# Performance work log

Hardware: AMD Instinct MI355X
Metric: run time of the kernel (lower is better)

## Reference

```python
import jax, jax.numpy as jnp
import numpy as np

EPS = 1e-6


def gaussian_filt(x, k, sigma):
    # x: [B,H,W,C]; depthwise gaussian conv with reflect padding, matching
    # TCFormer guassian_filt (kernel uses analytic 1/(2*pi*var) normalization).
    C = x.shape[-1]
    coords = jnp.arange(k, dtype=x.dtype)
    mean = (k - 1) / 2.0
    var = float(sigma) ** 2
    g1 = jnp.exp(-(coords - mean) ** 2 / (2.0 * var))
    gk = (g1[:, None] * g1[None, :]) / (2.0 * np.pi * var)  # [k,k]
    w = jnp.tile(gk[:, :, None, None], (1, 1, 1, C))  # HWIO, depthwise
    pad = (k - 1) // 2
    xp = jnp.pad(x, ((0, 0), (pad, pad), (pad, pad), (0, 0)), mode='reflect')
    return jax.lax.conv_general_dilated(
        xp, w, (1, 1), 'VALID',
        dimension_numbers=('NHWC', 'HWIO', 'NHWC'), feature_group_count=C)


def token2map(x, loc, H, W, kernel_size, sigma):
    # Scatter-mean tokens x [B,N,C] at normalized locations loc [B,N,2] in [-1,1]
    # onto an HxW grid, then gaussian-splat to fill holes. Returns NHWC map.
    B, N, C = x.shape
    loc = jnp.clip(loc, -1.0, 1.0)
    px = jnp.clip(jnp.round(0.5 * (loc[..., 0] + 1.0) * W - 0.5).astype(jnp.int32), 0, W - 1)
    py = jnp.clip(jnp.round(0.5 * (loc[..., 1] + 1.0) * H - 0.5).astype(jnp.int32), 0, H - 1)
    idx = py * W + px + jnp.arange(B, dtype=jnp.int32)[:, None] * (H * W)  # [B,N]
    src = jnp.concatenate([x, jnp.ones((B, N, 1), x.dtype)], axis=-1)  # [B,N,C+1]
    out = jnp.zeros((B * H * W, C + 1), x.dtype).at[idx.reshape(-1)].add(src.reshape(-1, C + 1))
    out = out.reshape(B, H, W, C + 1)
    feat, cnt = out[..., :C], out[..., C:]
    feat = feat / (cnt + EPS)
    mask = (cnt > 0).astype(x.dtype)
    feat = feat * mask
    if kernel_size > 1:
        # reconstruct_feature: fill empty cells with gaussian-interpolated values
        y = gaussian_filt(jnp.concatenate([feat, mask], axis=-1), kernel_size, sigma)
        fi, mi = y[..., :C], y[..., C:]
        fi = fi / (mi + EPS)
        fi = fi * (mi > 0).astype(x.dtype)
        feat = feat + (1.0 - mask) * fi
    return feat  # [B,H,W,C]


def layernorm(x, g, b, eps=1e-5):
    m = jnp.mean(x, axis=-1, keepdims=True)
    v = jnp.var(x, axis=-1, keepdims=True)
    return (x - m) / jnp.sqrt(v + eps) * g + b


def setup_inputs() -> dict:
    key = jax.random.key(0)
    ks = jax.random.split(key, 8)
    B, N, C, H, W = 8, 16384, 64, 128, 128
    SR = 8
    std = 0.02
    return {
        'x': jax.random.normal(ks[0], (B, N, C), jnp.float32),
        'x_source': jax.random.normal(ks[1], (B, N, C), jnp.float32),
        'loc_source': jax.random.uniform(ks[2], (B, N, 2), jnp.float32) * 2.0 - 1.0,
        'conf_source': jax.random.normal(ks[3], (B, N, 1), jnp.float32) * 0.1,
        'q_w': jax.random.normal(ks[4], (C, C), jnp.float32) * std,
        'kv_w': jax.random.normal(ks[5], (2 * C, C), jnp.float32) * std,
        'sr_w': jax.random.normal(ks[6], (SR, SR, C, C), jnp.float32) * np.sqrt(2.0 / (SR * SR * C)),
        'sr_b': jnp.zeros((C,), jnp.float32),
        'norm_w': jnp.ones((C,), jnp.float32),
        'norm_b': jnp.zeros((C,), jnp.float32),
        'proj_w': jax.random.normal(ks[7], (C, C), jnp.float32) * std,
        'proj_b': jnp.zeros((C,), jnp.float32),
        'H': H,
        'W': W,
    }


def reference(x, x_source, loc_source, conf_source, q_w, kv_w, sr_w, sr_b,
              norm_w, norm_b, proj_w, proj_b, H, W):
    B, N, C = x.shape
    num_heads = 1  # PVT stage-1
    hd = C // num_heads
    scale = hd ** -0.5
    sr = sr_w.shape[0]  # sr_ratio = 8

    # q projection: [B, nh, N, hd]
    q = (x @ q_w.T).reshape(B, N, num_heads, hd).transpose(0, 2, 1, 3)

    # token2map scatter-splat (kernel = sr_ratio + 1, sigma = 2)
    feat = token2map(x_source, loc_source, H, W, sr + 1, 2.0)  # [B,H,W,C]

    # SR conv (k = stride = sr_ratio), then layernorm
    xs = jax.lax.conv_general_dilated(
        feat, sr_w, (sr, sr), 'VALID',
        dimension_numbers=('NHWC', 'HWIO', 'NHWC')) + sr_b
    h, w = H // sr, W // sr
    xs = layernorm(xs.reshape(B, h * w, C), norm_w, norm_b)  # [B,M,C]

    # confidence map on the reduced grid (kernel_size=1 => pure scatter-mean)
    conf = token2map(conf_source, loc_source, h, w, 1, 1.0).reshape(B, h * w)  # [B,M]

    kv = (xs @ kv_w.T).reshape(B, h * w, 2, num_heads, hd)
    k = kv[:, :, 0].transpose(0, 2, 1, 3)  # [B,nh,M,hd]
    v = kv[:, :, 1].transpose(0, 2, 1, 3)

    attn = jnp.einsum('bhnd,bhmd->bhnm', q, k) * scale
    attn = attn + conf[:, None, None, :]  # additive confidence bias
    attn = jax.nn.softmax(attn, axis=-1)
    out = jnp.einsum('bhnm,bhmd->bhnd', attn, v)
    out = out.transpose(0, 2, 1, 3).reshape(B, N, C)
    return out @ proj_w.T + proj_b
```

## Files before the change

### kernel.cpp

```cpp
#include <hip/hip_runtime.h>
#include <hip/hip_bf16.h>

#define NN 16384
#define NC 64
#define GH 128
#define GW 128
#define GM 256

typedef __attribute__((ext_vector_type(8))) short bf16x8;
typedef __attribute__((ext_vector_type(4))) float f32x4;

static __device__ __forceinline__ int reflect128(int i){
  if (i < 0) i = -i;
  if (i > 127) i = 254 - i;
  return i;
}

static __device__ __forceinline__ ushort f2bf(float f){
  __hip_bfloat16 h = __float2bfloat16(f);
  union { __hip_bfloat16 h; ushort u; } v; v.h = h;
  return v.u;
}

static __device__ __forceinline__ int cell_of(float l, float S2, int hi){
  l = fminf(fmaxf(l, -1.f), 1.f);
  float u = l + 1.f;
  int p = (int)rintf(u*S2 - 0.5f);
  return min(max(p,0),hi);
}

__global__ __launch_bounds__(256) void k_zero(float4* __restrict__ p, int n4){
  int i = blockIdx.x*256 + threadIdx.x;
  int stride = gridDim.x*256;
  float4 z = make_float4(0.f,0.f,0.f,0.f);
  for (; i < n4; i += stride) p[i] = z;
}

__global__ __launch_bounds__(256) void k_scatter_feat(
    const float* __restrict__ xsrc, const float* __restrict__ loc,
    float* __restrict__ featg){
  int gid = blockIdx.x*256 + threadIdx.x;
  int t = gid >> 6;
  int b = t >> 14;
  int px = cell_of(loc[2*t],   64.f, 127);
  int py = cell_of(loc[2*t+1], 64.f, 127);
  int cell = (b*GH + py)*GW + px;
  atomicAdd(&featg[cell*NC + (gid & 63)], xsrc[gid]);
}

__global__ __launch_bounds__(256) void k_scatter_aux(
    const float* __restrict__ loc, const float* __restrict__ csrc,
    float* __restrict__ cnt, float* __restrict__ csum, float* __restrict__ ccnt){
  int t = blockIdx.x*256 + threadIdx.x;
  int b = t >> 14;
  int px = cell_of(loc[2*t],   64.f, 127);
  int py = cell_of(loc[2*t+1], 64.f, 127);
  atomicAdd(&cnt[(b*GH+py)*GW+px], 1.0f);
  int qx = cell_of(loc[2*t],   8.f, 15);
  int qy = cell_of(loc[2*t+1], 8.f, 15);
  int cell = b*GM + qy*16 + qx;
  atomicAdd(&csum[cell], csrc[t]);
  atomicAdd(&ccnt[cell], 1.0f);
}

__global__ __launch_bounds__(256) void k_finalize_feat(
    float* __restrict__ featg, const float* __restrict__ cnt){
  int gid = blockIdx.x*256 + threadIdx.x;
  float cn = cnt[gid>>6];
  float v  = featg[gid];
  featg[gid] = (cn > 0.f) ? v/(cn+1e-6f) : 0.f;
}

__global__ __launch_bounds__(256) void k_finalize_conf(
    const float* __restrict__ csum, const float* __restrict__ ccnt,
    float* __restrict__ conf){
  int i = blockIdx.x*256 + threadIdx.x;
  float cn = ccnt[i];
  conf[i] = (cn > 0.f) ? csum[i]/(cn+1e-6f) : 0.f;
}

__global__ __launch_bounds__(256) void k_fill2(
    const float* __restrict__ cnt, float* __restrict__ feat){
  int gid = blockIdx.x*256 + threadIdx.x;
  int p = gid >> 2, cg = gid & 3;
  if (cnt[p] > 0.f) return;
  int b = p>>14, py=(p>>7)&127, px=p&127;
  const float fn = 0.039788735772973836f;
  float g1[9];
  #pragma unroll
  for (int i=0;i<9;++i){ float d=(float)i-4.f; g1[i]=__expf(-d*d*0.125f); }
  float4 acc[4];
  #pragma unroll
  for (int i=0;i<4;++i) acc[i]=make_float4(0.f,0.f,0.f,0.f);
  float msum=0.f;
  for (int dy=0; dy<9; ++dy){
    int iy = reflect128(py-4+dy);
    for (int dx=0; dx<9; ++dx){
      int ix = reflect128(px-4+dx);
      int q  = (b*GH+iy)*GW+ix;
      if (cnt[q] <= 0.f) continue;
      float wn = g1[dy]*g1[dx]*fn;
      msum += wn;
      const float4* fr = (const float4*)&feat[q*NC + cg*16];
      #pragma unroll
      for (int k=0;k<4;++k){
        float4 vv = fr[k];
        acc[k].x += wn*vv.x; acc[k].y += wn*vv.y;
        acc[k].z += wn*vv.z; acc[k].w += wn*vv.w;
      }
    }
  }
  if (msum <= 0.f) return;
  float inv = 1.f/(msum + 1e-6f);
  float4* o = (float4*)&feat[p*NC + cg*16];
  #pragma unroll
  for (int k=0;k<4;++k)
    o[k] = make_float4(acc[k].x*inv, acc[k].y*inv, acc[k].z*inv, acc[k].w*inv);
}

static __device__ __forceinline__ int rowswz(int bid){
  return ((bid & 7) << 7) + (bid >> 3);
}

__global__ __launch_bounds__(256) void k_finfillh(
    float* __restrict__ feat, const float* __restrict__ cnt,
    float* __restrict__ feath, float* __restrict__ maskh){
  __shared__ float F[GW*NC];
  __shared__ float CR[GW];
  int py = rowswz(blockIdx.x), t = threadIdx.x;
  const float fn = 0.039788735772973836f;
  float g1n[9];
  #pragma unroll
  for (int i=0;i<9;++i){ float d=(float)i-4.f; g1n[i]=__expf(-d*d*0.125f)*fn; }
  if (t < GW) CR[t] = cnt[py*GW + t];
  __syncthreads();
  for (int i=t*4; i<GW*NC; i+=1024){
    int px = i>>6;
    float cn = CR[px];
    float inv = (cn > 0.f) ? 1.f/(cn+1e-6f) : 0.f;
    float4 v = *(const float4*)&feat[(size_t)py*GW*NC + i];
    v.x*=inv; v.y*=inv; v.z*=inv; v.w*=inv;
    *(float4*)&F[i] = v;
    *(float4*)&feat[(size_t)py*GW*NC + i] = v;
  }
  __syncthreads();
  for (int i=t*4; i<GW*NC; i+=1024){
    int px = i>>6, c = i&63;
    float4 acc = make_float4(0.f,0.f,0.f,0.f);
    #pragma unroll
    for (int dx=0; dx<9; ++dx){
      int ix = reflect128(px-4+dx);
      float w = g1n[dx];
      float4 v = *(const float4*)&F[ix*NC + c];
      acc.x += w*v.x; acc.y += w*v.y; acc.z += w*v.z; acc.w += w*v.w;
    }
    *(float4*)&feath[(size_t)py*GW*NC + i] = acc;
  }
  if (t < GW){
    float hm = 0.f;
    #pragma unroll
    for (int dx=0; dx<9; ++dx){
      int ix = reflect128(t-4+dx);
      hm += g1n[dx]*((CR[ix] > 0.f) ? 1.f : 0.f);
    }
    maskh[py*GW + t] = hm;
  }
}

__global__ __launch_bounds__(256) void k_fillv(
    float* __restrict__ feat, const float* __restrict__ cnt,
    const float* __restrict__ feath, const float* __restrict__ maskh){
  int pyg = rowswz(blockIdx.x), t = threadIdx.x;
  int b = pyg >> 7, pyl = pyg & 127;
  int px = t>>1, c0 = (t&1)<<5;
  float g1[9];
  #pragma unroll
  for (int i=0;i<9;++i){ float d=(float)i-4.f; g1[i]=__expf(-d*d*0.125f); }
  float cn = cnt[pyg*GW + px];
  float ym = 0.f;
  int ry[9];
  #pragma unroll
  for (int dy=0; dy<9; ++dy){
    ry[dy] = b*GH + reflect128(pyl-4+dy);
    ym += g1[dy]*maskh[ry[dy]*GW + px];
  }
  if (cn > 0.f || ym <= 0.f) return;
  float inv = 1.f/(ym + 1e-6f);
  float4 acc[8];
  #pragma unroll
  for (int k=0;k<8;++k) acc[k]=make_float4(0.f,0.f,0.f,0.f);
  #pragma unroll
  for (int dy=0; dy<9; ++dy){
    float w = g1[dy];
    const float4* hf = (const float4*)&feath[((size_t)ry[dy]*GW+px)*NC + c0];
    #pragma unroll
    for (int k=0;k<8;++k){
      float4 v = hf[k];
      acc[k].x += w*v.x; acc[k].y += w*v.y; acc[k].z += w*v.z; acc[k].w += w*v.w;
    }
  }
  float4* o = (float4*)&feat[((size_t)pyg*GW+px)*NC + c0];
  #pragma unroll
  for (int k=0;k<8;++k)
    o[k] = make_float4(acc[k].x*inv, acc[k].y*inv, acc[k].z*inv, acc[k].w*inv);
}

__global__ __launch_bounds__(256) void k_srconv(
    const float* __restrict__ feat, const float* __restrict__ srw,
    float* __restrict__ xs0){
  alignas(16) __shared__ float A[64*65];
  alignas(16) __shared__ float Bs[64*64];
  int mt = blockIdx.x, kh = blockIdx.y;
  int t = threadIdx.x;
  int tm = t>>4, tn = t&15;
  float acc[4][4] = {{0.f}};
  for (int kc=0; kc<8; ++kc){
    __syncthreads();
    for (int idx=t; idx<4096; idx+=256){
      int mr = idx>>6, kk = idx&63;
      int m = mt*64+mr;
      int b = m>>8, oh=(m>>4)&15, ow=m&15;
      A[mr*65+kk] = feat[(((b*GH)+(oh*8+kh))*GW + ow*8)*NC + kc*64 + kk];
    }
    for (int idx=t; idx<4096; idx+=256)
      Bs[idx] = srw[(kh*512 + kc*64)*64 + idx];
    __syncthreads();
    for (int kk=0; kk<64; ++kk){
      float4 bv = *(const float4*)&Bs[kk*64 + tn*4];
      #pragma unroll
      for (int i=0;i<4;++i){
        float av = A[(tm*4+i)*65 + kk];
        acc[i][0] += av*bv.x; acc[i][1] += av*bv.y;
        acc[i][2] += av*bv.z; acc[i][3] += av*bv.w;
      }
    }
  }
  #pragma unroll
  for (int i=0;i<4;++i)
    #pragma unroll
    for (int j=0;j<4;++j)
      atomicAdd(&xs0[(mt*64+tm*4+i)*64 + tn*4+j], acc[i][j]);
}

__global__ __launch_bounds__(256) void k_srconv2(
    const float* __restrict__ feat, const float* __restrict__ srw,
    float* __restrict__ part){
  alignas(16) __shared__ float A[64*65];
  alignas(16) __shared__ float Bs[64*64];
  int mt = blockIdx.x, kh = blockIdx.y, kq = blockIdx.z;
  int t = threadIdx.x;
  int tm = t>>4, tn = t&15;
  float acc[4][4] = {{0.f}};
  for (int kc=0; kc<4; ++kc){
    int kw = kq*4 + kc;
    __syncthreads();
    for (int idx=t; idx<4096; idx+=256){
      int mr = idx>>6, kk = idx&63;
      int m = mt*64+mr;
      int b = m>>8, oh=(m>>4)&15, ow=m&15;
      A[mr*65+kk] = feat[(((b*GH)+(oh*8+kh))*GW + ow*8 + kw)*NC + kk];
    }
    for (int idx=t; idx<4096; idx+=256)
      Bs[idx] = srw[(kh*512 + kw*64)*64 + idx];
    __syncthreads();
    for (int kk=0; kk<64; ++kk){
      float4 bv = *(const float4*)&Bs[kk*64 + tn*4];
      #pragma unroll
      for (int i=0;i<4;++i){
        float av = A[(tm*4+i)*65 + kk];
        acc[i][0] += av*bv.x; acc[i][1] += av*bv.y;
        acc[i][2] += av*bv.z; acc[i][3] += av*bv.w;
      }
    }
  }
  float* pdst = part + (size_t)(kh*2+kq)*2048*64;
  #pragma unroll
  for (int i=0;i<4;++i)
    #pragma unroll
    for (int j=0;j<4;++j)
      pdst[(mt*64+tm*4+i)*64 + tn*4+j] = acc[i][j];
}

__global__ __launch_bounds__(256) void k_ln(
    const float* __restrict__ xs0, const float* __restrict__ srb,
    const float* __restrict__ nw, const float* __restrict__ nbv,
    float* __restrict__ xs){
  int row  = blockIdx.x*4 + (threadIdx.x>>6);
  int lane = threadIdx.x & 63;
  float v = xs0[row*64+lane] + srb[lane];
  float s = v;
  #pragma unroll
  for (int off=32; off; off>>=1) s += __shfl_xor(s, off, 64);
  float mean = s*(1.f/64.f);
  float d = v - mean;
  float s2 = d*d;
  #pragma unroll
  for (int off=32; off; off>>=1) s2 += __shfl_xor(s2, off, 64);
  float var = s2*(1.f/64.f);
  xs[row*64+lane] = d*(1.f/sqrtf(var+1e-5f))*nw[lane] + nbv[lane];
}

__global__ __launch_bounds__(256) void k_kv1(
    const float* __restrict__ xs, const float* __restrict__ kvw,
    float* __restrict__ kraw, float* __restrict__ vraw){
  int gid = blockIdx.x*256 + threadIdx.x;
  int r = gid >> 6, d = gid & 63;
  const float* xr = &xs[r*64];
  float ka=0.f, va=0.f;
  for (int c=0;c<64;++c){
    float xc = xr[c];
    ka += xc*kvw[d*64+c];
    va += xc*kvw[(64+d)*64+c];
  }
  kraw[gid] = ka;
  vraw[gid] = va;
}

__global__ __launch_bounds__(256) void k_kvproj2(
    const float* __restrict__ kraw, const float* __restrict__ vraw,
    const float* __restrict__ qw, const float* __restrict__ pw,
    ushort* __restrict__ KB, ushort* __restrict__ VB){
  int gid = blockIdx.x*256 + threadIdx.x;
  int r = gid >> 6, c = gid & 63;
  int b = r >> 8, m = r & 255;
  const float* kr = &kraw[r*64];
  const float* vr = &vraw[r*64];
  float ak=0.f, av=0.f;
  for (int i=0;i<64;++i){
    ak += kr[i]*qw[i*64+c];
    av += vr[i]*pw[c*64+i];
  }
  {
    int nt = m>>4, l15 = m&15, kb = c>>5, h = (c>>3)&3, j = c&7;
    KB[((((b*16 + nt)*2 + kb)*4 + h)*16 + l15)*8 + j] = f2bf(ak);
  }
  {
    int ct = c>>4, n15 = c&15, kb2 = m>>5, h2 = (m>>3)&3, j2 = m&7;
    VB[((((b*4 + ct)*8 + kb2)*4 + h2)*16 + n15)*8 + j2] = f2bf(av);
  }
}

__global__ __launch_bounds__(256) void k_kvfused(
    const float* __restrict__ part, const float* __restrict__ srb,
    const float* __restrict__ nw, const float* __restrict__ nbv,
    const float* __restrict__ kvw, const float* __restrict__ qw,
    const float* __restrict__ pw,
    ushort* __restrict__ KB, ushort* __restrict__ VB){
  __shared__ float XR[4][64], KR[4][64], VR[4][64];
  int t = threadIdx.x;
  int rl = t>>6, d = t&63;
  int r  = blockIdx.x*4 + rl;
  float v = srb[d];
  #pragma unroll
  for (int ps=0; ps<16; ++ps)
    v += part[(size_t)ps*2048*64 + r*64 + d];
  float s = v;
  #pragma unroll
  for (int off=32; off; off>>=1) s += __shfl_xor(s, off, 64);
  float mean = s*(1.f/64.f);
  float dd = v - mean;
  float s2 = dd*dd;
  #pragma unroll
  for (int off=32; off; off>>=1) s2 += __shfl_xor(s2, off, 64);
  float var = s2*(1.f/64.f);
  XR[rl][d] = dd*(1.f/sqrtf(var+1e-5f))*nw[d] + nbv[d];
  __syncthreads();
  float ka=0.f, va=0.f;
  for (int cc=0; cc<64; ++cc){
    float xc = XR[rl][cc];
    ka += xc*kvw[d*64+cc];
    va += xc*kvw[(64+d)*64+cc];
  }
  KR[rl][d] = ka; VR[rl][d] = va;
  __syncthreads();
  int c = d;
  float ak=0.f, av=0.f;
  for (int i=0;i<64;++i){
    ak += KR[rl][i]*qw[i*64+c];
    av += VR[rl][i]*pw[c*64+i];
  }
  int b = r>>8, m = r&255;
  {
    int nt = m>>4, l15 = m&15, kb = c>>5, h = (c>>3)&3, j = c&7;
    KB[((((b*16 + nt)*2 + kb)*4 + h)*16 + l15)*8 + j] = f2bf(ak);
  }
  {
    int ct = c>>4, n15 = c&15, kb2 = m>>5, h2 = (m>>3)&3, j2 = m&7;
    VB[((((b*4 + ct)*8 + kb2)*4 + h2)*16 + n15)*8 + j2] = f2bf(av);
  }
}

__global__ __launch_bounds__(256) void k_attn5(
    const float* __restrict__ x, const ushort* __restrict__ KB,
    const ushort* __restrict__ VB, const float* __restrict__ conf,
    const float* __restrict__ projb, float* __restrict__ out){
  alignas(16) __shared__ ushort P[4*4096];
  int t = threadIdx.x, w = t>>6, l = t&63;
  int b = blockIdx.x >> 8;
  int row0 = ((blockIdx.x & 255) << 6) + (w<<4);
  int l15 = l & 15, h = l >> 4;
  const ushort* KBb = KB + b*16384;
  const ushort* VBb = VB + b*16384;
  bf16x8 xa[2];
  {
    const float* xr = x + (size_t)(b*NN + row0 + l15)*64 + h*8;
    #pragma unroll
    for (int kb=0; kb<2; ++kb){
      float4 a0 = *(const float4*)(xr + 32*kb);
      float4 a1 = *(const float4*)(xr + 32*kb + 4);
      bf16x8 v;
      v[0]=(short)f2bf(a0.x); v[1]=(short)f2bf(a0.y);
      v[2]=(short)f2bf(a0.z); v[3]=(short)f2bf(a0.w);
      v[4]=(short)f2bf(a1.x); v[5]=(short)f2bf(a1.y);
      v[6]=(short)f2bf(a1.z); v[7]=(short)f2bf(a1.w);
      xa[kb]=v;
    }
  }
  f32x4 acc[16];
  #pragma unroll
  for (int nt=0;nt<16;++nt) acc[nt] = (f32x4){0.f,0.f,0.f,0.f};
  #pragma unroll
  for (int nt=0;nt<16;++nt){
    bf16x8 b0 = *(const bf16x8*)(KBb + (nt*2+0)*512 + l*8);
    bf16x8 b1 = *(const bf16x8*)(KBb + (nt*2+1)*512 + l*8);
    acc[nt] = __builtin_amdgcn_mfma_f32_16x16x32_bf16(xa[0], b0, acc[nt], 0,0,0);
    acc[nt] = __builtin_amdgcn_mfma_f32_16x16x32_bf16(xa[1], b1, acc[nt], 0,0,0);
  }
  float rs[4] = {0.f,0.f,0.f,0.f};
  ushort* Pw = P + w*4096;
  #pragma unroll
  for (int nt=0;nt<16;++nt){
    float cf = conf[b*GM + nt*16 + l15];
    #pragma unroll
    for (int reg=0;reg<4;++reg){
      float p = __expf(fmaf(acc[nt][reg], 0.125f, cf));
      rs[reg] += p;
      int m   = nt*16 + l15;
      int row = h*4 + reg;
      int ld  = ((m>>3)&3)*16 + row;
      int idx = ((m>>5)*512 + ld*8 + (m&7)) ^ (ld & 0x38);
      Pw[idx] = f2bf(p);
    }
  }
  #pragma unroll
  for (int off=1; off<16; off<<=1){
    #pragma unroll
    for (int reg=0;reg<4;++reg) rs[reg] += __shfl_xor(rs[reg], off, 64);
  }
  f32x4 oacc[4];
  #pragma unroll
  for (int ct=0;ct<4;++ct) oacc[ct] = (f32x4){0.f,0.f,0.f,0.f};
  #pragma unroll
  for (int kb2=0;kb2<8;++kb2){
    int ridx = (kb2*512 + l*8) ^ (l & 0x38);
    bf16x8 pa = *(const bf16x8*)(Pw + ridx);
    #pragma unroll
    for (int ct=0;ct<4;++ct){
      bf16x8 vb = *(const bf16x8*)(VBb + (ct*8+kb2)*512 + l*8);
      oacc[ct] = __builtin_amdgcn_mfma_f32_16x16x32_bf16(pa, vb, oacc[ct], 0,0,0);
    }
  }
  float* OT = (float*)Pw;
  #pragma unroll
  for (int ct=0;ct<4;++ct){
    float pb4 = projb[ct*16 + l15];
    #pragma unroll
    for (int reg=0;reg<4;++reg)
      OT[(h*4+reg)*68 + ct*16 + l15] = oacc[ct][reg]/rs[reg] + pb4;
  }
  #pragma unroll
  for (int i=0;i<4;++i){
    int row = i*4 + h;
    float4 v = *(const float4*)&OT[row*68 + l15*4];
    *(float4*)&out[(size_t)(b*NN + row0 + row)*64 + l15*4] = v;
  }
}

__global__ __launch_bounds__(256) void k_attn6(
    const float* __restrict__ x, const ushort* __restrict__ KB,
    const ushort* __restrict__ VB, const float* __restrict__ conf,
    const float* __restrict__ projb, float* __restrict__ out){
  alignas(16) __shared__ ushort P[4*4096];
  int t = threadIdx.x, w = t>>6, l = t&63;
  int b = blockIdx.x >> 8;
  int row0 = ((blockIdx.x & 255) << 6) + (w<<4);
  int l15 = l & 15, h = l >> 4;
  const ushort* KBb = KB + b*16384;
  const ushort* VBb = VB + b*16384;

  bf16x8 xa[2];
  {
    const float* xr = x + (size_t)(b*NN + row0 + l15)*64 + h*8;
    #pragma unroll
    for (int kb=0; kb<2; ++kb){
      float4 a0 = *(const float4*)(xr + 32*kb);
      float4 a1 = *(const float4*)(xr + 32*kb + 4);
      bf16x8 v;
      v[0]=(short)f2bf(a0.x); v[1]=(short)f2bf(a0.y);
      v[2]=(short)f2bf(a0.z); v[3]=(short)f2bf(a0.w);
      v[4]=(short)f2bf(a1.x); v[5]=(short)f2bf(a1.y);
      v[6]=(short)f2bf(a1.z); v[7]=(short)f2bf(a1.w);
      xa[kb]=v;
    }
  }

  float rs[4] = {0.f,0.f,0.f,0.f};
  f32x4 oacc[4];
  #pragma unroll
  for (int ct=0;ct<4;++ct) oacc[ct] = (f32x4){0.f,0.f,0.f,0.f};
  ushort* Pw = P + w*4096;

  #pragma unroll
  for (int c=0;c<4;++c){
    f32x4 acc[4];
    #pragma unroll
    for (int q=0;q<4;++q) acc[q] = (f32x4){0.f,0.f,0.f,0.f};
    #pragma unroll
    for (int q=0;q<4;++q){
      int nt = c*4 + q;
      bf16x8 b0 = *(const bf16x8*)(KBb + (nt*2+0)*512 + l*8);
      bf16x8 b1 = *(const bf16x8*)(KBb + (nt*2+1)*512 + l*8);
      acc[q] = __builtin_amdgcn_mfma_f32_16x16x32_bf16(xa[0], b0, acc[q], 0,0,0);
      acc[q] = __builtin_amdgcn_mfma_f32_16x16x32_bf16(xa[1], b1, acc[q], 0,0,0);
    }
    #pragma unroll
    for (int q=0;q<4;++q){
      int nt = c*4 + q;
      float cf = conf[b*GM + nt*16 + l15];
      #pragma unroll
      for (int reg=0;reg<4;++reg){
        float p = __expf(fmaf(acc[q][reg], 0.125f, cf));
        rs[reg] += p;
        int m   = nt*16 + l15;
        int row = h*4 + reg;
        int ld  = ((m>>3)&3)*16 + row;
        int idx = ((m>>5)*512 + ld*8 + (m&7)) ^ (ld & 0x38);
        Pw[idx] = f2bf(p);
      }
    }
    #pragma unroll
    for (int kk=0;kk<2;++kk){
      int kb2 = c*2 + kk;
      int ridx = (kb2*512 + l*8) ^ (l & 0x38);
      bf16x8 pa = *(const bf16x8*)(Pw + ridx);
      #pragma unroll
      for (int ct=0;ct<4;++ct){
        bf16x8 vb = *(const bf16x8*)(VBb + (ct*8+kb2)*512 + l*8);
        oacc[ct] = __builtin_amdgcn_mfma_f32_16x16x32_bf16(pa, vb, oacc[ct], 0,0,0);
      }
    }
  }

  #pragma unroll
  for (int off=1; off<16; off<<=1){
    #pragma unroll
    for (int reg=0;reg<4;++reg) rs[reg] += __shfl_xor(rs[reg], off, 64);
  }

  float* OT = (float*)Pw;
  #pragma unroll
  for (int ct=0;ct<4;++ct){
    float pb4 = projb[ct*16 + l15];
    #pragma unroll
    for (int reg=0;reg<4;++reg)
      OT[(h*4+reg)*68 + ct*16 + l15] = oacc[ct][reg]/rs[reg] + pb4;
  }
  #pragma unroll
  for (int i=0;i<4;++i){
    int row = i*4 + h;
    float4 v = *(const float4*)&OT[row*68 + l15*4];
    *(float4*)&out[(size_t)(b*NN + row0 + row)*64 + l15*4] = v;
  }
}

extern "C" void kernel_launch(void* const* d_in, const int* in_sizes, int n_in,
                              void* d_out, int out_size, void* d_ws, size_t ws_size,
                              hipStream_t stream){
  const float* x    = (const float*)d_in[0];
  const float* xsrc = (const float*)d_in[1];
  const float* loc  = (const float*)d_in[2];
  const float* csrc = (const float*)d_in[3];
  const float* qw   = (const float*)d_in[4];
  const float* kvw  = (const float*)d_in[5];
  const float* srw  = (const float*)d_in[6];
  const float* srb  = (const float*)d_in[7];
  const float* nw   = (const float*)d_in[8];
  const float* nbv  = (const float*)d_in[9];
  const float* pw   = (const float*)d_in[10];
  const float* pb   = (const float*)d_in[11];
  float* out = (float*)d_out;
  float* ws = (float*)d_ws;

  size_t of_feat  = 0;
  size_t of_cnt   = of_feat  + 8ull*GH*GW*NC;
  size_t of_csum  = of_cnt   + 8ull*GH*GW;
  size_t of_ccnt  = of_csum  + 8ull*GM;
  size_t zero_end = of_ccnt  + 8ull*GM;
  size_t of_feath = zero_end;
  size_t of_maskh = of_feath + 8ull*GH*GW*NC;
  size_t of_part  = of_maskh + 8ull*GH*GW;
  size_t of_conf  = of_part  + 16ull*2048*64;
  size_t of_kb    = of_conf  + 8ull*GM;
  size_t of_vb    = of_kb    + 8ull*8192;
  size_t total_p  = of_vb    + 8ull*8192;

  if (ws_size >= total_p*sizeof(float)){
    k_zero         <<<2048,        256, 0, stream>>>((float4*)ws, (int)(zero_end>>2));
    k_scatter_feat <<<8*NN*NC/256, 256, 0, stream>>>(xsrc, loc, ws+of_feat);
    k_scatter_aux  <<<8*NN/256,    256, 0, stream>>>(loc, csrc, ws+of_cnt, ws+of_csum, ws+of_ccnt);
    k_finalize_conf<<<8*GM/256,    256, 0, stream>>>(ws+of_csum, ws+of_ccnt, ws+of_conf);
    k_finfillh     <<<8*GH,        256, 0, stream>>>(ws+of_feat, ws+of_cnt, ws+of_feath, ws+of_maskh);
    k_fillv        <<<8*GH,        256, 0, stream>>>(ws+of_feat, ws+of_cnt, ws+of_feath, ws+of_maskh);
    dim3 gconv(32, 8, 2);
    k_srconv2      <<<gconv,       256, 0, stream>>>(ws+of_feat, srw, ws+of_part);
    k_kvfused      <<<8*GM/4,      256, 0, stream>>>(ws+of_part, srb, nw, nbv, kvw, qw, pw,
                                                     (ushort*)(ws+of_kb), (ushort*)(ws+of_vb));
    k_attn6        <<<8*NN/64,     256, 0, stream>>>(x, (const ushort*)(ws+of_kb),
                                                     (const ushort*)(ws+of_vb),
                                                     ws+of_conf, pb, out);
  } else {
    size_t f_feat = 0;
    size_t f_cnt  = f_feat + 8ull*GH*GW*NC;
    size_t f_csum = f_cnt  + 8ull*GH*GW;
    size_t f_ccnt = f_csum + 8ull*GM;
    size_t f_xs0  = f_ccnt + 8ull*GM;
    size_t f_zero = f_xs0  + 8ull*GM*NC;
    size_t f_conf = f_zero;
    size_t f_xs   = f_conf + 8ull*GM;
    size_t f_kr   = f_xs   + 8ull*GM*NC;
    size_t f_vr   = f_kr   + 8ull*GM*NC;
    size_t f_kb   = f_vr   + 8ull*GM*NC;
    size_t f_vb   = f_kb   + 8ull*8192;
    hipMemsetAsync(ws, 0, f_zero*sizeof(float), stream);
    k_scatter_feat <<<8*NN*NC/256, 256, 0, stream>>>(xsrc, loc, ws+f_feat);
    k_scatter_aux  <<<8*NN/256,    256, 0, stream>>>(loc, csrc, ws+f_cnt, ws+f_csum, ws+f_ccnt);
    k_finalize_feat<<<8*GH*GW*NC/256, 256, 0, stream>>>(ws+f_feat, ws+f_cnt);
    k_finalize_conf<<<8*GM/256,    256, 0, stream>>>(ws+f_csum, ws+f_ccnt, ws+f_conf);
    k_fill2        <<<8*GH*GW*4/256, 256, 0, stream>>>(ws+f_cnt, ws+f_feat);
    dim3 gconv(8*GM/64, 8);
    k_srconv       <<<gconv,       256, 0, stream>>>(ws+f_feat, srw, ws+f_xs0);
    k_ln           <<<8*GM/4,      256, 0, stream>>>(ws+f_xs0, srb, nw, nbv, ws+f_xs);
    k_kv1          <<<8*GM*NC/256, 256, 0, stream>>>(ws+f_xs, kvw, ws+f_kr, ws+f_vr);
    k_kvproj2      <<<8*GM*NC/256, 256, 0, stream>>>(ws+f_kr, ws+f_vr, qw, pw,
                                                     (ushort*)(ws+f_kb), (ushort*)(ws+f_vb));
    k_attn5        <<<8*NN/64,     256, 0, stream>>>(x, (const ushort*)(ws+f_kb),
                                                     (const ushort*)(ws+f_vb),
                                                     ws+f_conf, pb, out);
  }
}
```

Before: 184.0 us.

## Fuse aux scatter and conf finalize into neighbors; shrink attention blocks to one wave

Merges the count/confidence scatter into the per-channel feature scatter kernel, using lanes c==0..2 for the auxiliary atomics. Folds confidence finalization into the KV projection kernel. Splits the attention kernel into single-wave 64-thread blocks with a private 8KB LDS buffer so more blocks can be scheduled. Together these remove two kernel launches and their dependent gaps, at the cost of some divergence in the scatter kernel.

Result: slower. 257.0 us (+39.7%).

```diff
diff --git a/kernel.cpp b/kernel.cpp
--- a/kernel.cpp
+++ b/kernel.cpp
@@ -34,6 +34,30 @@
   int stride = gridDim.x*256;
   float4 z = make_float4(0.f,0.f,0.f,0.f);
   for (; i < n4; i += stride) p[i] = z;
+}
+
+__global__ __launch_bounds__(256) void k_scatter_feat2(
+    const float* __restrict__ xsrc, const float* __restrict__ loc,
+    const float* __restrict__ csrc, float* __restrict__ featg,
+    float* __restrict__ cnt, float* __restrict__ csum, float* __restrict__ ccnt){
+  int gid = blockIdx.x*256 + threadIdx.x;
+  int t = gid >> 6, c = gid & 63;
+  int b = t >> 14;
+  int px = cell_of(loc[2*t],   64.f, 127);
+  int py = cell_of(loc[2*t+1], 64.f, 127);
+  int cell = (b*GH + py)*GW + px;
+  atomicAdd(&featg[cell*NC + c], xsrc[gid]);
+  if (c == 0){
+    atomicAdd(&cnt[cell], 1.0f);
+  } else if (c == 1){
+    int qx = cell_of(loc[2*t],   8.f, 15);
+    int qy = cell_of(loc[2*t+1], 8.f, 15);
+    atomicAdd(&csum[b*GM + qy*16 + qx], csrc[t]);
+  } else if (c == 2){
+    int qx = cell_of(loc[2*t],   8.f, 15);
+    int qy = cell_of(loc[2*t+1], 8.f, 15);
+    atomicAdd(&ccnt[b*GM + qy*16 + qx], 1.0f);
+  }
 }
 
 __global__ __launch_bounds__(256) void k_scatter_feat(
@@ -340,6 +364,62 @@
   }
 }
 
+__global__ __launch_bounds__(256) void k_kvfused2(
+    const float* __restrict__ part, const float* __restrict__ srb,
+    const float* __restrict__ nw, const float* __restrict__ nbv,
+    const float* __restrict__ kvw, const float* __restrict__ qw,
+    const float* __restrict__ pw,
+    const float* __restrict__ csum, const float* __restrict__ ccnt,
+    float* __restrict__ conf,
+    ushort* __restrict__ KB, ushort* __restrict__ VB){
+  __shared__ float XR[4][64], KR[4][64], VR[4][64];
+  int t = threadIdx.x;
+  int rl = t>>6, d = t&63;
+  int r  = blockIdx.x*4 + rl;
+  if (d == 0){
+    float cn = ccnt[r];
+    conf[r] = (cn > 0.f) ? csum[r]/(cn+1e-6f) : 0.f;
+  }
+  float v = srb[d];
+  #pragma unroll
+  for (int ps=0; ps<16; ++ps)
+    v += part[(size_t)ps*2048*64 + r*64 + d];
+  float s = v;
+  #pragma unroll
+  for (int off=32; off; off>>=1) s += __shfl_xor(s, off, 64);
+  float mean = s*(1.f/64.f);
+  float dd = v - mean;
+  float s2 = dd*dd;
+  #pragma unroll
+  for (int off=32; off; off>>=1) s2 += __shfl_xor(s2, off, 64);
+  float var = s2*(1.f/64.f);
+  XR[rl][d] = dd*(1.f/sqrtf(var+1e-5f))*nw[d] + nbv[d];
+  __syncthreads();
+  float ka=0.f, va=0.f;
+  for (int cc=0; cc<64; ++cc){
+    float xc = XR[rl][cc];
+    ka += xc*kvw[d*64+cc];
+    va += xc*kvw[(64+d)*64+cc];
+  }
+  KR[rl][d] = ka; VR[rl][d] = va;
+  __syncthreads();
+  int c = d;
+  float ak=0.f, av=0.f;
+  for (int i=0;i<64;++i){
+    ak += KR[rl][i]*qw[i*64+c];
+    av += VR[rl][i]*pw[c*64+i];
+  }
+  int b = r>>8, m = r&255;
+  {
+    int nt = m>>4, l15 = m&15, kb = c>>5, h = (c>>3)&3, j = c&7;
+    KB[((((b*16 + nt)*2 + kb)*4 + h)*16 + l15)*8 + j] = f2bf(ak);
+  }
+  {
+    int ct = c>>4, n15 = c&15, kb2 = m>>5, h2 = (m>>3)&3, j2 = m&7;
+    VB[((((b*4 + ct)*8 + kb2)*4 + h2)*16 + n15)*8 + j2] = f2bf(av);
+  }
+}
+
 __global__ __launch_bounds__(256) void k_kvfused(
     const float* __restrict__ part, const float* __restrict__ srb,
     const float* __restrict__ nw, const float* __restrict__ nbv,
@@ -476,14 +556,14 @@
   }
 }
 
-__global__ __launch_bounds__(256) void k_attn6(
+__global__ __launch_bounds__(64) void k_attn8(
     const float* __restrict__ x, const ushort* __restrict__ KB,
     const ushort* __restrict__ VB, const float* __restrict__ conf,
     const float* __restrict__ projb, float* __restrict__ out){
-  alignas(16) __shared__ ushort P[4*4096];
-  int t = threadIdx.x, w = t>>6, l = t&63;
-  int b = blockIdx.x >> 8;
-  int row0 = ((blockIdx.x & 255) << 6) + (w<<4);
+  alignas(16) __shared__ ushort Pw[4096];
+  int l = threadIdx.x;
+  int b = blockIdx.x >> 10;
+  int row0 = (blockIdx.x & 1023) << 4;
   int l15 = l & 15, h = l >> 4;
   const ushort* KBb = KB + b*16384;
   const ushort* VBb = VB + b*16384;
@@ -508,7 +588,6 @@
   f32x4 oacc[4];
   #pragma unroll
   for (int ct=0;ct<4;++ct) oacc[ct] = (f32x4){0.f,0.f,0.f,0.f};
-  ushort* Pw = P + w*4096;
 
   #pragma unroll
   for (int c=0;c<4;++c){
@@ -605,19 +684,19 @@
   size_t total_p  = of_vb    + 8ull*8192;
 
   if (ws_size >= total_p*sizeof(float)){
-    k_zero         <<<2048,        256, 0, stream>>>((float4*)ws, (int)(zero_end>>2));
-    k_scatter_feat <<<8*NN*NC/256, 256, 0, stream>>>(xsrc, loc, ws+of_feat);
-    k_scatter_aux  <<<8*NN/256,    256, 0, stream>>>(loc, csrc, ws+of_cnt, ws+of_csum, ws+of_ccnt);
-    k_finalize_conf<<<8*GM/256,    256, 0, stream>>>(ws+of_csum, ws+of_ccnt, ws+of_conf);
-    k_finfillh     <<<8*GH,        256, 0, stream>>>(ws+of_feat, ws+of_cnt, ws+of_feath, ws+of_maskh);
-    k_fillv        <<<8*GH,        256, 0, stream>>>(ws+of_feat, ws+of_cnt, ws+of_feath, ws+of_maskh);
+    k_zero          <<<2048,        256, 0, stream>>>((float4*)ws, (int)(zero_end>>2));
+    k_scatter_feat2 <<<8*NN*NC/256, 256, 0, stream>>>(xsrc, loc, csrc, ws+of_feat,
+                                                      ws+of_cnt, ws+of_csum, ws+of_ccnt);
+    k_finfillh      <<<8*GH,        256, 0, stream>>>(ws+of_feat, ws+of_cnt, ws+of_feath, ws+of_maskh);
+    k_fillv         <<<8*GH,        256, 0, stream>>>(ws+of_feat, ws+of_cnt, ws+of_feath, ws+of_maskh);
     dim3 gconv(32, 8, 2);
-    k_srconv2      <<<gconv,       256, 0, stream>>>(ws+of_feat, srw, ws+of_part);
-    k_kvfused      <<<8*GM/4,      256, 0, stream>>>(ws+of_part, srb, nw, nbv, kvw, qw, pw,
-                                                     (ushort*)(ws+of_kb), (ushort*)(ws+of_vb));
-    k_attn6        <<<8*NN/64,     256, 0, stream>>>(x, (const ushort*)(ws+of_kb),
-                                                     (const ushort*)(ws+of_vb),
-                                                     ws+of_conf, pb, out);
+    k_srconv2       <<<gconv,       256, 0, stream>>>(ws+of_feat, srw, ws+of_part);
+    k_kvfused2      <<<8*GM/4,      256, 0, stream>>>(ws+of_part, srb, nw, nbv, kvw, qw, pw,
+                                                      ws+of_csum, ws+of_ccnt, ws+of_conf,
+                                                      (ushort*)(ws+of_kb), (ushort*)(ws+of_vb));
+    k_attn8         <<<8*NN/16,     64,  0, stream>>>(x, (const ushort*)(ws+of_kb),
+                                                      (const ushort*)(ws+of_vb),
+                                                      ws+of_conf, pb, out);
   } else {
     size_t f_feat = 0;
     size_t f_cnt  = f_feat + 8ull*GH*GW*NC;
```
